# Kernel tuning notes

Measured on AMD Instinct MI355X. Metric: run time of the kernel, lower is better.

Reference implementation:

```python
import jax, jax.numpy as jnp
import numpy as np

NUM_HEADS = 16
ROPE_THETA = 10000.0
SCALE_FACTOR = 1.0  # max_position_embeddings / block_size


def _rope_cos_sin(T, head_dim, dtype):
    # standard RoPE frequencies: inv_freq_i = theta^(-2i/d)
    inv_freq = 1.0 / (ROPE_THETA ** (jnp.arange(0, head_dim, 2, dtype=jnp.float32) / head_dim))
    pos = jnp.arange(T, dtype=jnp.float32) / SCALE_FACTOR
    ang = pos[:, None] * inv_freq[None, :]            # (T, D/2)
    ang = jnp.concatenate([ang, ang], axis=-1)        # (T, D)
    return jnp.cos(ang).astype(dtype)[None, None], jnp.sin(ang).astype(dtype)[None, None]


def _rotate_half(u):
    d = u.shape[-1] // 2
    return jnp.concatenate([-u[..., d:], u[..., :d]], axis=-1)


def setup_inputs() -> dict:
    key = jax.random.key(0)
    ks = jax.random.split(key, 5)
    B, T, C = 2, 2048, 1024
    x = jax.random.normal(ks[0], (B, T, C), dtype=jnp.float32)
    Wqkv = jax.random.normal(ks[1], (C, 3 * C), dtype=jnp.float32) * (1.0 / np.sqrt(C))
    bqkv = jnp.zeros((3 * C,), dtype=jnp.float32)
    Wproj = jax.random.normal(ks[2], (C, C), dtype=jnp.float32) * (1.0 / np.sqrt(C))
    bproj = jnp.zeros((C,), dtype=jnp.float32)
    return {"x": x, "Wqkv": Wqkv, "bqkv": bqkv, "Wproj": Wproj, "bproj": bproj}


def reference(x, Wqkv, bqkv, Wproj, bproj):
    B, T, C = x.shape
    H = NUM_HEADS
    D = C // H
    qkv = x @ Wqkv + bqkv                              # (B, T, 3C)
    q, k, v = jnp.split(qkv, 3, axis=-1)
    # (B, H, T, D)
    q = q.reshape(B, T, H, D).transpose(0, 2, 1, 3)
    k = k.reshape(B, T, H, D).transpose(0, 2, 1, 3)
    v = v.reshape(B, T, H, D).transpose(0, 2, 1, 3)
    cos, sin = _rope_cos_sin(T, D, x.dtype)
    q = q * cos + _rotate_half(q) * sin
    k = k * cos + _rotate_half(k) * sin
    att = jnp.einsum('bhtd,bhsd->bhts', q, k) / jnp.sqrt(jnp.asarray(D, x.dtype))
    causal = jnp.tril(jnp.ones((T, T), dtype=bool))
    att = jnp.where(causal[None, None], att, jnp.asarray(-jnp.inf, att.dtype))
    att = jax.nn.softmax(att, axis=-1)
    y = jnp.einsum('bhts,bhsd->bhtd', att, v)          # (B, H, T, D)
    y = y.transpose(0, 2, 1, 3).reshape(B, T, C)
    return y @ Wproj + bproj
```

## Files before the change

kernel.cpp:

```cpp
#include <hip/hip_runtime.h>
#include <hip/hip_bf16.h>

typedef __hip_bfloat16 bf16;
typedef __attribute__((ext_vector_type(8))) __bf16 bf16x8;
typedef __attribute__((ext_vector_type(4))) __bf16 bf16x4;
typedef __attribute__((ext_vector_type(4))) float f32x4;
typedef unsigned short u16;

#define MFMA16(a, b, c) __builtin_amdgcn_mfma_f32_16x16x32_bf16((a), (b), (c), 0, 0, 0)

static constexpr int B_ = 2, T_ = 2048, C_ = 1024, H_ = 16, D_ = 64;
static constexpr int BT = B_ * T_;
static constexpr int N3 = 3 * C_;

__device__ __forceinline__ void gload16(void* lds, const void* g) {
    __builtin_amdgcn_global_load_lds(
        (const __attribute__((address_space(1))) unsigned int*)g,
        (__attribute__((address_space(3))) unsigned int*)lds, 16, 0, 0);
}

__device__ __forceinline__ u16 bb(float x) {
    return __builtin_bit_cast(u16, __float2bfloat16(x));
}


__global__ void k_transpose_w(const float* __restrict__ src, bf16* __restrict__ dst,
                              int K, int N) {
    __shared__ float t[32][33];
    int bx = blockIdx.x * 32;
    int by = blockIdx.y * 32;
    int tx = threadIdx.x & 31, ty = threadIdx.x >> 5;
#pragma unroll
    for (int i = 0; i < 32; i += 8)
        t[ty + i][tx] = src[(size_t)(by + ty + i) * N + bx + tx];
    __syncthreads();
#pragma unroll
    for (int i = 0; i < 32; i += 8)
        dst[(size_t)(bx + ty + i) * K + by + tx] = __float2bfloat16(t[tx][ty + i]);
}

__global__ void k_convert_x(const float* __restrict__ src, bf16* __restrict__ dst, int n4) {
    int i = blockIdx.x * 256 + threadIdx.x;
    if (i >= n4) return;
    float4 v = reinterpret_cast<const float4*>(src)[i];
    dst[4 * i + 0] = __float2bfloat16(v.x);
    dst[4 * i + 1] = __float2bfloat16(v.y);
    dst[4 * i + 2] = __float2bfloat16(v.z);
    dst[4 * i + 3] = __float2bfloat16(v.w);
}

__global__ void k_rope_table(float* __restrict__ ct, float* __restrict__ st) {
    int i = blockIdx.x * 256 + threadIdx.x;
    if (i >= T_ * 32) return;
    int t = i >> 5, f = i & 31;
    float invf = exp2f(-(float)f * 0.4152410118609203f);
    float ang = (float)t * invf;
    ct[i] = cosf(ang);
    st[i] = sinf(ang);
}

__global__ __launch_bounds__(256) void k_gemm_qkv(
    const bf16* __restrict__ A, const bf16* __restrict__ Bt,
    const float* __restrict__ bias,
    const float* __restrict__ ct, const float* __restrict__ st,
    bf16* __restrict__ q, bf16* __restrict__ kk, bf16* __restrict__ vt) {
    __shared__ bf16 lA[2][128 * 32];
    __shared__ bf16 lB[2][128 * 32];
    const int tid = threadIdx.x;
    const int wave = tid >> 6, lane = tid & 63;
    const int wm = wave >> 1, wn = wave & 1;
    const int l16 = lane & 15, lg = lane >> 4;
    const int m0 = blockIdx.y * 128, n0 = blockIdx.x * 128;

    f32x4 acc[4][4];
#pragma unroll
    for (int i = 0; i < 4; i++)
#pragma unroll
        for (int j = 0; j < 4; j++) acc[i][j] = (f32x4){0.f, 0.f, 0.f, 0.f};

    const int r = lane >> 2;
    const int sc = (lane & 3) ^ (r & 3);
    const bf16* gA = A + (size_t)(m0 + wave * 32 + r) * 1024 + sc * 8;
    const bf16* gB = Bt + (size_t)(n0 + wave * 32 + r) * 1024 + sc * 8;
    const int sw = (lg ^ (l16 & 3)) * 8;

    auto stage = [&](int buf, int k0) {
        bf16* sA = lA[buf] + wave * 1024;
        bf16* sB = lB[buf] + wave * 1024;
        gload16(sA, gA + k0);
        gload16(sA + 512, gA + (size_t)16 * 1024 + k0);
        gload16(sB, gB + k0);
        gload16(sB + 512, gB + (size_t)16 * 1024 + k0);
    };

    stage(0, 0);
    int buf = 0;
    for (int k0 = 0; k0 < 1024; k0 += 32) {
        __syncthreads();
        if (k0 + 32 < 1024) stage(buf ^ 1, k0 + 32);
        bf16x8 af[4], bfr[4];
#pragma unroll
        for (int mi = 0; mi < 4; mi++)
            af[mi] = *(const bf16x8*)(lA[buf] + (wm * 64 + mi * 16 + l16) * 32 + sw);
#pragma unroll
        for (int nj = 0; nj < 4; nj++)
            bfr[nj] = *(const bf16x8*)(lB[buf] + (wn * 64 + nj * 16 + l16) * 32 + sw);
#pragma unroll
        for (int mi = 0; mi < 4; mi++)
#pragma unroll
            for (int nj = 0; nj < 4; nj++)
                acc[mi][nj] = MFMA16(af[mi], bfr[nj], acc[mi][nj]);
        buf ^= 1;
    }

    const int b = m0 >> 11;
#pragma unroll
    for (int mi = 0; mi < 4; mi++) {
        int mbase = m0 + wm * 64 + mi * 16 + lg * 4;
#pragma unroll
        for (int nj = 0; nj < 4; nj++) {
            int n = n0 + wn * 64 + nj * 16 + l16;
            int which = n >> 10;
            int nq = n & 1023;
            int h = nq >> 6, d = nq & 63;
#pragma unroll
            for (int rr = 0; rr < 4; rr++) {
                int m = mbase + rr;
                int t = m & 2047;
                float v = acc[mi][nj][rr] + bias[n];
                if (which == 2) {
                    vt[((size_t)(b * 16 + h) * 64 + d) * 2048 + t] = __float2bfloat16(v);
                } else {
                    float pv = acc[mi][nj ^ 2][rr] + bias[n ^ 32];
                    float c = ct[t * 32 + (d & 31)];
                    float s = st[t * 32 + (d & 31)];
                    float rh = (d < 32) ? -pv : pv;
                    float o = v * c + rh * s;
                    bf16* dst = (which == 0) ? q : kk;
                    dst[((size_t)(b * 16 + h) * 2048 + t) * 64 + d] = __float2bfloat16(o);
                }
            }
        }
    }
}

__global__ __launch_bounds__(128, 3) void k_attn(
    const bf16* __restrict__ qg, const bf16* __restrict__ kg,
    const bf16* __restrict__ vtg, bf16* __restrict__ y) {
    __shared__ bf16 lk[2][32 * 64];
    __shared__ bf16 lv[2][64 * 32];
    const int wv = threadIdx.x >> 6;
    const int lane = threadIdx.x & 63;
    const int l16 = lane & 15, lg = lane >> 4;
    const int id = blockIdx.x;
    const int bh = id & 31;
    const int strip = 31 - (id >> 5);
    const int q0w = strip * 64 + 32 * wv;
    const bf16* qh = qg + (size_t)bh * (2048 * 64);
    const bf16* kh = kg + (size_t)bh * (2048 * 64);
    const bf16* vh = vtg + (size_t)bh * (64 * 2048);

    bf16x8 qf[2][2];
#pragma unroll
    for (int g = 0; g < 2; g++)
#pragma unroll
        for (int h = 0; h < 2; h++)
            qf[g][h] = *(const bf16x8*)(qh + (size_t)(q0w + 16 * g + l16) * 64 + 32 * h + 8 * lg);

    f32x4 o[2][4];
#pragma unroll
    for (int g = 0; g < 2; g++)
#pragma unroll
        for (int dt = 0; dt < 4; dt++) o[g][dt] = (f32x4){0.f, 0.f, 0.f, 0.f};
    float mm[2] = {-1e30f, -1e30f}, ls[2] = {0.f, 0.f};

    auto stage = [&](int buf, int kt) {
#pragma unroll
        for (int i = 0; i < 2; i++) {
            int cc = 2 * wv + i;
            {
                int row = 8 * cc + (lane >> 3);
                int sc = (lane & 7) ^ (lane >> 3);
                gload16(&lk[buf][cc * 512], kh + (size_t)(kt + row) * 64 + sc * 8);
            }
            {
                int row = 16 * cc + (lane >> 2);
                int sc = (lane & 3) ^ ((lane >> 2) & 3);
                gload16(&lv[buf][cc * 512], vh + (size_t)row * 2048 + kt + sc * 8);
            }
        }
    };

    const f32x4 z = (f32x4){0.f, 0.f, 0.f, 0.f};
    auto compute = [&](int buf, bool diag) {
        bf16x8 kf2[2][2];
#pragma unroll
        for (int t = 0; t < 2; t++)
#pragma unroll
            for (int h = 0; h < 2; h++) {
                int krow = 16 * t + l16;
                int koff = ((h * 64 + lg * 16) ^ ((l16 & 7) << 4)) >> 1;
                kf2[t][h] = *(const bf16x8*)(&lk[buf][krow * 64 + koff]);
            }
        bf16x8 vf[4];
#pragma unroll
        for (int dt = 0; dt < 4; dt++) {
            int vrow = 16 * dt + l16;
            int s4 = (l16 & 3) << 4;
            const bf16* vb = &lv[buf][vrow * 32];
            bf16x4 lo = *(const bf16x4*)(vb + (((lg * 8) ^ s4) >> 1));
            bf16x4 hi = *(const bf16x4*)(vb + (((32 + lg * 8) ^ s4) >> 1));
            vf[dt] = __builtin_shufflevector(lo, hi, 0, 1, 2, 3, 4, 5, 6, 7);
        }
        f32x4 s[2][2];
#pragma unroll
        for (int g = 0; g < 2; g++)
#pragma unroll
            for (int t = 0; t < 2; t++) {
                f32x4 acc = MFMA16(kf2[t][0], qf[g][0], z);
                s[g][t] = MFMA16(kf2[t][1], qf[g][1], acc);
            }
#pragma unroll
        for (int g = 0; g < 2; g++) {
            float p[8];
#pragma unroll
            for (int t = 0; t < 2; t++)
#pragma unroll
                for (int rr = 0; rr < 4; rr++) {
                    float v = s[g][t][rr] * 0.125f;
                    if (diag && (16 * t + 4 * lg + rr > 16 * g + l16)) v = -1e30f;
                    p[4 * t + rr] = v;
                }
            float pm = p[0];
#pragma unroll
            for (int i = 1; i < 8; i++) pm = fmaxf(pm, p[i]);
            pm = fmaxf(pm, __shfl_xor(pm, 16, 64));
            pm = fmaxf(pm, __shfl_xor(pm, 32, 64));
            float mn = fmaxf(mm[g], pm);
            float al = __expf(mm[g] - mn);
#pragma unroll
            for (int dt = 0; dt < 4; dt++) o[g][dt] *= al;
            ls[g] *= al;
            mm[g] = mn;
            float ps = 0.f;
#pragma unroll
            for (int i = 0; i < 8; i++) {
                p[i] = __expf(p[i] - mn);
                ps += p[i];
            }
            ls[g] += ps;
            bf16x8 pf;
#pragma unroll
            for (int j = 0; j < 8; j++)
                pf[j] = __builtin_bit_cast(__bf16, __float2bfloat16(p[j]));
#pragma unroll
            for (int dt = 0; dt < 4; dt++) o[g][dt] = MFMA16(vf[dt], pf, o[g][dt]);
        }
    };

    const int nt = 2 * strip + 2;
    stage(0, 0);
    for (int it = 0; it < nt; ++it) {
        __syncthreads();
        if (it + 1 < nt) stage((it + 1) & 1, 32 * (it + 1));
        int kt = 32 * it;
        if (kt <= q0w) compute(it & 1, kt == q0w);
    }

    const int b = bh >> 4, h = bh & 15;
#pragma unroll
    for (int g = 0; g < 2; g++) {
        float lt = ls[g];
        lt += __shfl_xor(lt, 16, 64);
        lt += __shfl_xor(lt, 32, 64);
        float inv = 1.f / lt;
        bf16* yp = y + ((size_t)(b * 2048 + q0w + 16 * g + l16)) * 1024 + h * 64 + 4 * lg;
#pragma unroll
        for (int dt = 0; dt < 4; dt++) {
            *(ushort4*)(yp + 16 * dt) = make_ushort4(
                bb(o[g][dt][0] * inv), bb(o[g][dt][1] * inv),
                bb(o[g][dt][2] * inv), bb(o[g][dt][3] * inv));
        }
    }
}

__global__ __launch_bounds__(256) void k_gemm_proj(
    const bf16* __restrict__ A, const bf16* __restrict__ Bt,
    const float* __restrict__ bias, float* __restrict__ out) {
    __shared__ bf16 lA[2][128 * 32];
    __shared__ bf16 lB[2][128 * 32];
    const int tid = threadIdx.x;
    const int wave = tid >> 6, lane = tid & 63;
    const int wm = wave >> 1, wn = wave & 1;
    const int l16 = lane & 15, lg = lane >> 4;
    const int m0 = blockIdx.y * 128, n0 = blockIdx.x * 128;

    f32x4 acc[4][4];
#pragma unroll
    for (int i = 0; i < 4; i++)
#pragma unroll
        for (int j = 0; j < 4; j++) acc[i][j] = (f32x4){0.f, 0.f, 0.f, 0.f};

    const int r = lane >> 2;
    const int sc = (lane & 3) ^ (r & 3);
    const bf16* gA = A + (size_t)(m0 + wave * 32 + r) * 1024 + sc * 8;
    const bf16* gB = Bt + (size_t)(n0 + wave * 32 + r) * 1024 + sc * 8;
    const int sw = (lg ^ (l16 & 3)) * 8;

    auto stage = [&](int buf, int k0) {
        bf16* sA = lA[buf] + wave * 1024;
        bf16* sB = lB[buf] + wave * 1024;
        gload16(sA, gA + k0);
        gload16(sA + 512, gA + (size_t)16 * 1024 + k0);
        gload16(sB, gB + k0);
        gload16(sB + 512, gB + (size_t)16 * 1024 + k0);
    };

    stage(0, 0);
    int buf = 0;
    for (int k0 = 0; k0 < 1024; k0 += 32) {
        __syncthreads();
        if (k0 + 32 < 1024) stage(buf ^ 1, k0 + 32);
        bf16x8 af[4], bfr[4];
#pragma unroll
        for (int mi = 0; mi < 4; mi++)
            af[mi] = *(const bf16x8*)(lA[buf] + (wm * 64 + mi * 16 + l16) * 32 + sw);
#pragma unroll
        for (int nj = 0; nj < 4; nj++)
            bfr[nj] = *(const bf16x8*)(lB[buf] + (wn * 64 + nj * 16 + l16) * 32 + sw);
#pragma unroll
        for (int mi = 0; mi < 4; mi++)
#pragma unroll
            for (int nj = 0; nj < 4; nj++)
                acc[mi][nj] = MFMA16(af[mi], bfr[nj], acc[mi][nj]);
        buf ^= 1;
    }

#pragma unroll
    for (int mi = 0; mi < 4; mi++) {
        int mbase = m0 + wm * 64 + mi * 16 + lg * 4;
#pragma unroll
        for (int nj = 0; nj < 4; nj++) {
            int n = n0 + wn * 64 + nj * 16 + l16;
#pragma unroll
            for (int rr = 0; rr < 4; rr++) {
                out[(size_t)(mbase + rr) * 1024 + n] = acc[mi][nj][rr] + bias[n];
            }
        }
    }
}

extern "C" void kernel_launch(void* const* d_in, const int* in_sizes, int n_in,
                              void* d_out, int out_size, void* d_ws, size_t ws_size,
                              hipStream_t stream) {
    const float* x = (const float*)d_in[0];
    const float* Wqkv = (const float*)d_in[1];
    const float* bqkv = (const float*)d_in[2];
    const float* Wproj = (const float*)d_in[3];
    const float* bproj = (const float*)d_in[4];
    float* out = (float*)d_out;

    char* ws = (char*)d_ws;
    bf16* xb = (bf16*)ws;      ws += (size_t)BT * C_ * 2;
    bf16* wqkvT = (bf16*)ws;   ws += (size_t)N3 * C_ * 2;
    bf16* wprojT = (bf16*)ws;  ws += (size_t)C_ * C_ * 2;
    bf16* qb = (bf16*)ws;      ws += (size_t)B_ * H_ * T_ * D_ * 2;
    bf16* kb = (bf16*)ws;      ws += (size_t)B_ * H_ * T_ * D_ * 2;
    bf16* vtb = (bf16*)ws;     ws += (size_t)B_ * H_ * T_ * D_ * 2;
    bf16* yb = (bf16*)ws;      ws += (size_t)BT * C_ * 2;
    float* ct = (float*)ws;    ws += (size_t)T_ * 32 * 4;
    float* st = (float*)ws;    ws += (size_t)T_ * 32 * 4;

    hipLaunchKernelGGL(k_transpose_w, dim3(N3 / 32, C_ / 32), dim3(256), 0, stream,
                       Wqkv, wqkvT, C_, N3);
    hipLaunchKernelGGL(k_transpose_w, dim3(C_ / 32, C_ / 32), dim3(256), 0, stream,
                       Wproj, wprojT, C_, C_);
    hipLaunchKernelGGL(k_convert_x, dim3((BT * C_ / 4) / 256), dim3(256), 0, stream,
                       x, xb, BT * C_ / 4);
    hipLaunchKernelGGL(k_rope_table, dim3((T_ * 32) / 256), dim3(256), 0, stream, ct, st);
    hipLaunchKernelGGL(k_gemm_qkv, dim3(N3 / 128, BT / 128), dim3(256), 0, stream,
                       xb, wqkvT, bqkv, ct, st, qb, kb, vtb);
    hipLaunchKernelGGL(k_attn, dim3(32 * 32), dim3(128), 0, stream,
                       qb, kb, vtb, yb);
    hipLaunchKernelGGL(k_gemm_proj, dim3(C_ / 128, BT / 128), dim3(256), 0, stream,
                       yb, wprojT, bproj, out);
}
```

Baseline: 156.6 us.

## Split attention KV range across two wave pairs and merge partial softmax

The attention block grows from 2 to 4 waves. Two wave pairs each process half of the causal key range for the same 64-query strip, with separate double-buffered LDS staging. The partial max, sum and output accumulators are then merged through LDS with the online-softmax rescale. This roughly halves the serial KV loop per block and increases parallelism, at the cost of extra LDS use, an extra merge and barrier, and higher register and occupancy pressure. The V tile swizzle is also changed to a different XOR pattern.

New measurement: 130.9 us. 16.4% less time.

```diff
diff --git a/kernel.cpp b/kernel.cpp
--- a/kernel.cpp
+++ b/kernel.cpp
@@ -144,19 +144,19 @@
     }
 }
 
-__global__ __launch_bounds__(128, 3) void k_attn(
+__global__ __launch_bounds__(256, 4) void k_attn(
     const bf16* __restrict__ qg, const bf16* __restrict__ kg,
     const bf16* __restrict__ vtg, bf16* __restrict__ y) {
-    __shared__ bf16 lk[2][32 * 64];
-    __shared__ bf16 lv[2][64 * 32];
+    __shared__ bf16 smem[2][2][4096];
     const int wv = threadIdx.x >> 6;
+    const int pair = wv >> 1, qh = wv & 1;
     const int lane = threadIdx.x & 63;
     const int l16 = lane & 15, lg = lane >> 4;
     const int id = blockIdx.x;
     const int bh = id & 31;
-    const int strip = 31 - (id >> 5);
-    const int q0w = strip * 64 + 32 * wv;
-    const bf16* qh = qg + (size_t)bh * (2048 * 64);
+    const int s = 31 - (id >> 5);
+    const int q0w = s * 64 + 32 * qh;
+    const bf16* qh_p = qg + (size_t)bh * (2048 * 64);
     const bf16* kh = kg + (size_t)bh * (2048 * 64);
     const bf16* vh = vtg + (size_t)bh * (64 * 2048);
 
@@ -165,7 +165,7 @@
     for (int g = 0; g < 2; g++)
 #pragma unroll
         for (int h = 0; h < 2; h++)
-            qf[g][h] = *(const bf16x8*)(qh + (size_t)(q0w + 16 * g + l16) * 64 + 32 * h + 8 * lg);
+            qf[g][h] = *(const bf16x8*)(qh_p + (size_t)(q0w + 16 * g + l16) * 64 + 32 * h + 8 * lg);
 
     f32x4 o[2][4];
 #pragma unroll
@@ -175,24 +175,28 @@
     float mm[2] = {-1e30f, -1e30f}, ls[2] = {0.f, 0.f};
 
     auto stage = [&](int buf, int kt) {
+        bf16* lk = &smem[pair][buf][0];
+        bf16* lv = &smem[pair][buf][2048];
 #pragma unroll
         for (int i = 0; i < 2; i++) {
-            int cc = 2 * wv + i;
+            int cc = 2 * qh + i;
             {
                 int row = 8 * cc + (lane >> 3);
-                int sc = (lane & 7) ^ (lane >> 3);
-                gload16(&lk[buf][cc * 512], kh + (size_t)(kt + row) * 64 + sc * 8);
+                int scc = (lane & 7) ^ (lane >> 3);
+                gload16(&lk[cc * 512], kh + (size_t)(kt + row) * 64 + scc * 8);
             }
             {
                 int row = 16 * cc + (lane >> 2);
-                int sc = (lane & 3) ^ ((lane >> 2) & 3);
-                gload16(&lv[buf][cc * 512], vh + (size_t)row * 2048 + kt + sc * 8);
+                int su = (lane & 3) ^ ((lane >> 3) & 3);
+                gload16(&lv[cc * 512], vh + (size_t)row * 2048 + kt + su * 8);
             }
         }
     };
 
     const f32x4 z = (f32x4){0.f, 0.f, 0.f, 0.f};
     auto compute = [&](int buf, bool diag) {
+        const bf16* lk = &smem[pair][buf][0];
+        const bf16* lv = &smem[pair][buf][2048];
         bf16x8 kf2[2][2];
 #pragma unroll
         for (int t = 0; t < 2; t++)
@@ -200,25 +204,25 @@
             for (int h = 0; h < 2; h++) {
                 int krow = 16 * t + l16;
                 int koff = ((h * 64 + lg * 16) ^ ((l16 & 7) << 4)) >> 1;
-                kf2[t][h] = *(const bf16x8*)(&lk[buf][krow * 64 + koff]);
+                kf2[t][h] = *(const bf16x8*)(&lk[krow * 64 + koff]);
             }
         bf16x8 vf[4];
 #pragma unroll
         for (int dt = 0; dt < 4; dt++) {
             int vrow = 16 * dt + l16;
-            int s4 = (l16 & 3) << 4;
-            const bf16* vb = &lv[buf][vrow * 32];
-            bf16x4 lo = *(const bf16x4*)(vb + (((lg * 8) ^ s4) >> 1));
-            bf16x4 hi = *(const bf16x4*)(vb + (((32 + lg * 8) ^ s4) >> 1));
+            int rs = (l16 >> 1) & 3;
+            const bf16* vb = &lv[vrow * 32];
+            bf16x4 lo = *(const bf16x4*)(vb + (((lg >> 1) ^ rs) * 8 + (lg & 1) * 4));
+            bf16x4 hi = *(const bf16x4*)(vb + (((2 + (lg >> 1)) ^ rs) * 8 + (lg & 1) * 4));
             vf[dt] = __builtin_shufflevector(lo, hi, 0, 1, 2, 3, 4, 5, 6, 7);
         }
-        f32x4 s[2][2];
+        f32x4 sg[2][2];
 #pragma unroll
         for (int g = 0; g < 2; g++)
 #pragma unroll
             for (int t = 0; t < 2; t++) {
                 f32x4 acc = MFMA16(kf2[t][0], qf[g][0], z);
-                s[g][t] = MFMA16(kf2[t][1], qf[g][1], acc);
+                sg[g][t] = MFMA16(kf2[t][1], qf[g][1], acc);
             }
 #pragma unroll
         for (int g = 0; g < 2; g++) {
@@ -227,7 +231,7 @@
             for (int t = 0; t < 2; t++)
 #pragma unroll
                 for (int rr = 0; rr < 4; rr++) {
-                    float v = s[g][t][rr] * 0.125f;
+                    float v = sg[g][t][rr] * 0.125f;
                     if (diag && (16 * t + 4 * lg + rr > 16 * g + l16)) v = -1e30f;
                     p[4 * t + rr] = v;
                 }
@@ -258,28 +262,59 @@
         }
     };
 
-    const int nt = 2 * strip + 2;
-    stage(0, 0);
-    for (int it = 0; it < nt; ++it) {
+    const int base = pair ? (s + 1) : 0;
+    const int niter = s + 1;
+    stage(0, 32 * base);
+    for (int i = 0; i < niter; ++i) {
         __syncthreads();
-        if (it + 1 < nt) stage((it + 1) & 1, 32 * (it + 1));
-        int kt = 32 * it;
-        if (kt <= q0w) compute(it & 1, kt == q0w);
-    }
-
-    const int b = bh >> 4, h = bh & 15;
-#pragma unroll
-    for (int g = 0; g < 2; g++) {
-        float lt = ls[g];
-        lt += __shfl_xor(lt, 16, 64);
-        lt += __shfl_xor(lt, 32, 64);
-        float inv = 1.f / lt;
-        bf16* yp = y + ((size_t)(b * 2048 + q0w + 16 * g + l16)) * 1024 + h * 64 + 4 * lg;
-#pragma unroll
-        for (int dt = 0; dt < 4; dt++) {
-            *(ushort4*)(yp + 16 * dt) = make_ushort4(
-                bb(o[g][dt][0] * inv), bb(o[g][dt][1] * inv),
-                bb(o[g][dt][2] * inv), bb(o[g][dt][3] * inv));
+        if (i + 1 < niter) stage((i + 1) & 1, 32 * (base + i + 1));
+        int kt = 32 * (base + i);
+        if (kt <= q0w) compute(i & 1, kt == q0w);
+    }
+
+    __syncthreads();
+    float* mg = (float*)&smem[0][0][0];
+    if (pair == 1) {
+        float* pp = mg + (qh * 64 + lane) * 36;
+        pp[0] = mm[0]; pp[1] = mm[1]; pp[2] = ls[0]; pp[3] = ls[1];
+#pragma unroll
+        for (int g = 0; g < 2; g++)
+#pragma unroll
+            for (int dt = 0; dt < 4; dt++)
+#pragma unroll
+                for (int rr = 0; rr < 4; rr++)
+                    pp[4 + g * 16 + dt * 4 + rr] = o[g][dt][rr];
+    }
+    __syncthreads();
+    if (pair == 0) {
+        const float* pp = mg + (qh * 64 + lane) * 36;
+#pragma unroll
+        for (int g = 0; g < 2; g++) {
+            float m1 = pp[g], l1 = pp[2 + g];
+            float mn = fmaxf(mm[g], m1);
+            float a0 = __expf(mm[g] - mn);
+            float a1 = __expf(m1 - mn);
+            ls[g] = ls[g] * a0 + l1 * a1;
+#pragma unroll
+            for (int dt = 0; dt < 4; dt++)
+#pragma unroll
+                for (int rr = 0; rr < 4; rr++)
+                    o[g][dt][rr] = o[g][dt][rr] * a0 + pp[4 + g * 16 + dt * 4 + rr] * a1;
+        }
+        const int b = bh >> 4, h = bh & 15;
+#pragma unroll
+        for (int g = 0; g < 2; g++) {
+            float lt = ls[g];
+            lt += __shfl_xor(lt, 16, 64);
+            lt += __shfl_xor(lt, 32, 64);
+            float inv = 1.f / lt;
+            bf16* yp = y + ((size_t)(b * 2048 + q0w + 16 * g + l16)) * 1024 + h * 64 + 4 * lg;
+#pragma unroll
+            for (int dt = 0; dt < 4; dt++) {
+                *(ushort4*)(yp + 16 * dt) = make_ushort4(
+                    bb(o[g][dt][0] * inv), bb(o[g][dt][1] * inv),
+                    bb(o[g][dt][2] * inv), bb(o[g][dt][3] * inv));
+            }
         }
     }
 }
@@ -380,7 +415,7 @@
     hipLaunchKernelGGL(k_rope_table, dim3((T_ * 32) / 256), dim3(256), 0, stream, ct, st);
     hipLaunchKernelGGL(k_gemm_qkv, dim3(N3 / 128, BT / 128), dim3(256), 0, stream,
                        xb, wqkvT, bqkv, ct, st, qb, kb, vtb);
-    hipLaunchKernelGGL(k_attn, dim3(32 * 32), dim3(128), 0, stream,
+    hipLaunchKernelGGL(k_attn, dim3(32 * 32), dim3(256), 0, stream,
                        qb, kb, vtb, yb);
     hipLaunchKernelGGL(k_gemm_proj, dim3(C_ / 128, BT / 128), dim3(256), 0, stream,
                        yb, wprojT, bproj, out);
```
